# Optimization experiments

Hardware: AMD Instinct MI355X
Metric: run time of the kernel (lower is better)

The kernel has to match this reference:

```python
import jax, jax.numpy as jnp
import numpy as np

TEMP = 0.1
EPS = 1e-8  # torch cosine_similarity eps
B, P, N, D = 256, 32, 512, 256


def setup_inputs() -> dict:
    key = jax.random.key(0)
    k1, k2, k3 = jax.random.split(key, 3)
    return {
        "anchors": jax.random.normal(k1, (B, D), dtype=jnp.float32),
        "positives": jax.random.normal(k2, (B, P, D), dtype=jnp.float32),
        "negatives": jax.random.normal(k3, (B, N, D), dtype=jnp.float32),
    }


def reference(anchors, positives, negatives):
    # all_samples: (B, K, D) with K = P + N
    all_samples = jnp.concatenate([positives, negatives], axis=1)
    # Cosine similarity of anchor vs every sample (the original broadcasts the
    # anchor over P identical rows; we compute the (B, K) row once).
    dots = jnp.einsum("bd,bkd->bk", anchors, all_samples)          # (B, K)
    na = jnp.linalg.norm(anchors, axis=-1, keepdims=True)           # (B, 1)
    nk = jnp.linalg.norm(all_samples, axis=-1)                      # (B, K)
    sim = dots / jnp.maximum(na * nk, EPS) / TEMP                   # (B, K)
    logp = jax.nn.log_softmax(sim, axis=-1)                         # (B, K)
    p = positives.shape[1]
    # labels = arange(P): gather picks -log_softmax at column p for row p;
    # since all P rows equal, this is just the first P columns of logp.
    return -jnp.mean(logp[:, :p])
```

## Files before the change

### kernel.cpp

```cpp
#include <hip/hip_runtime.h>
#include <math.h>

#define TEMP_INV 10.0f
#define EPS 1e-8f
#define B_ 256
#define P_ 32
#define N_ 512
#define D_ 256
#define K_ (P_ + N_)

__device__ __forceinline__ float wave_reduce_sum(float v) {
    #pragma unroll
    for (int m = 32; m >= 1; m >>= 1) v += __shfl_xor(v, m, 64);
    return v;
}

__device__ __forceinline__ float wave_reduce_max(float v) {
    #pragma unroll
    for (int m = 32; m >= 1; m >>= 1) v = fmaxf(v, __shfl_xor(v, m, 64));
    return v;
}

__global__ __launch_bounds__(256) void sim_kernel(
    const float* __restrict__ anchors,
    const float* __restrict__ positives,
    const float* __restrict__ negatives,
    float* __restrict__ sim) {
    int gw   = blockIdx.x * 4 + (threadIdx.x >> 6);
    int lane = threadIdx.x & 63;
    if (gw >= B_ * K_) return;
    int b = gw / K_;
    int k = gw - b * K_;

    const float4* a4 = (const float4*)(anchors + (size_t)b * D_);
    const float4* s4 = (k < P_)
        ? (const float4*)(positives + ((size_t)b * P_ + k) * D_)
        : (const float4*)(negatives + ((size_t)b * N_ + (k - P_)) * D_);

    float4 a = a4[lane];
    float4 s = s4[lane];

    float dot = a.x * s.x + a.y * s.y + a.z * s.z + a.w * s.w;
    float ss  = s.x * s.x + s.y * s.y + s.z * s.z + s.w * s.w;
    float aa  = a.x * a.x + a.y * a.y + a.z * a.z + a.w * a.w;

    dot = wave_reduce_sum(dot);
    ss  = wave_reduce_sum(ss);
    aa  = wave_reduce_sum(aa);

    if (lane == 0) {
        float denom = fmaxf(sqrtf(aa) * sqrtf(ss), EPS);
        sim[gw] = dot / denom * TEMP_INV;
    }
}

__global__ __launch_bounds__(256) void softmax_kernel(
    const float* __restrict__ sim,
    float* __restrict__ partials) {
    int b    = blockIdx.x;
    int tid  = threadIdx.x;
    int wid  = tid >> 6;
    int lane = tid & 63;
    const float* row = sim + (size_t)b * K_;

    float vals[3];
    int cnt = 0;
    float lmax = -INFINITY;
    for (int k = tid; k < K_; k += 256) {
        float v = row[k];
        vals[cnt++] = v;
        lmax = fmaxf(lmax, v);
    }

    __shared__ float s_max[4];
    __shared__ float s_sum[4];
    __shared__ float s_pos[4];

    float wmax = wave_reduce_max(lmax);
    if (lane == 0) s_max[wid] = wmax;
    __syncthreads();
    float bmax = fmaxf(fmaxf(s_max[0], s_max[1]), fmaxf(s_max[2], s_max[3]));

    float lsum = 0.0f;
    for (int i = 0; i < cnt; i++) lsum += expf(vals[i] - bmax);
    float wsum = wave_reduce_sum(lsum);
    if (lane == 0) s_sum[wid] = wsum;

    float lp = (tid < P_) ? vals[0] : 0.0f;
    float wp = wave_reduce_sum(lp);
    if (lane == 0) s_pos[wid] = wp;
    __syncthreads();

    if (tid == 0) {
        float bsum = s_sum[0] + s_sum[1] + s_sum[2] + s_sum[3];
        float bpos = s_pos[0] + s_pos[1] + s_pos[2] + s_pos[3];
        float lse  = bmax + logf(bsum);
        partials[b] = (float)P_ * lse - bpos;
    }
}

__global__ __launch_bounds__(256) void finalize_kernel(
    const float* __restrict__ partials,
    float* __restrict__ out) {
    int tid  = threadIdx.x;
    int wid  = tid >> 6;
    int lane = tid & 63;
    float v  = partials[tid];
    float ws = wave_reduce_sum(v);
    __shared__ float s[4];
    if (lane == 0) s[wid] = ws;
    __syncthreads();
    if (tid == 0) {
        out[0] = (s[0] + s[1] + s[2] + s[3]) / (float)(B_ * P_);
    }
}

extern "C" void kernel_launch(void* const* d_in, const int* in_sizes, int n_in,
                              void* d_out, int out_size, void* d_ws, size_t ws_size,
                              hipStream_t stream) {
    const float* anchors   = (const float*)d_in[0];
    const float* positives = (const float*)d_in[1];
    const float* negatives = (const float*)d_in[2];
    float* out      = (float*)d_out;
    float* sim      = (float*)d_ws;
    float* partials = sim + (size_t)B_ * K_;

    int n_rows   = B_ * K_;
    int n_blocks = (n_rows + 3) / 4;
    sim_kernel<<<n_blocks, 256, 0, stream>>>(anchors, positives, negatives, sim);
    softmax_kernel<<<B_, 256, 0, stream>>>(sim, partials);
    finalize_kernel<<<1, 256, 0, stream>>>(partials, out);
}
```

Before: 202.1 us.

## Process four samples per wave and fold finalize into softmax via atomics

Each wave now computes cosine similarity for four consecutive samples, loading the anchor once and issuing four independent row loads. This cuts the block count fourfold, reuses the anchor and its norm, and gives more memory-level parallelism per wave. The finalize kernel is removed: the sim kernel zeroes the output and each softmax block atomically adds its scaled partial. The atomic accumulation makes the float summation order nondeterministic.

```diff
diff --git a/kernel.cpp b/kernel.cpp
--- a/kernel.cpp
+++ b/kernel.cpp
@@ -8,6 +8,7 @@
 #define N_ 512
 #define D_ 256
 #define K_ (P_ + N_)
+#define G_ (K_ / 4)
 
 __device__ __forceinline__ float wave_reduce_sum(float v) {
     #pragma unroll
@@ -21,42 +22,59 @@
     return v;
 }
 
+__device__ __forceinline__ float dot4(float4 a, float4 b) {
+    return a.x * b.x + a.y * b.y + a.z * b.z + a.w * b.w;
+}
+
 __global__ __launch_bounds__(256) void sim_kernel(
     const float* __restrict__ anchors,
     const float* __restrict__ positives,
     const float* __restrict__ negatives,
-    float* __restrict__ sim) {
+    float* __restrict__ sim,
+    float* __restrict__ out) {
     int gw   = blockIdx.x * 4 + (threadIdx.x >> 6);
     int lane = threadIdx.x & 63;
-    if (gw >= B_ * K_) return;
-    int b = gw / K_;
-    int k = gw - b * K_;
+    int b  = gw / G_;
+    int g  = gw - b * G_;
+    int k0 = g * 4;
 
     const float4* a4 = (const float4*)(anchors + (size_t)b * D_);
-    const float4* s4 = (k < P_)
-        ? (const float4*)(positives + ((size_t)b * P_ + k) * D_)
-        : (const float4*)(negatives + ((size_t)b * N_ + (k - P_)) * D_);
+    float4 a = a4[lane];
 
-    float4 a = a4[lane];
-    float4 s = s4[lane];
+    const float4* base = (k0 < P_)
+        ? (const float4*)(positives + ((size_t)b * P_ + k0) * D_)
+        : (const float4*)(negatives + ((size_t)b * N_ + (k0 - P_)) * D_);
 
-    float dot = a.x * s.x + a.y * s.y + a.z * s.z + a.w * s.w;
-    float ss  = s.x * s.x + s.y * s.y + s.z * s.z + s.w * s.w;
-    float aa  = a.x * a.x + a.y * a.y + a.z * a.z + a.w * a.w;
+    float4 s0 = base[lane];
+    float4 s1 = base[64 + lane];
+    float4 s2 = base[128 + lane];
+    float4 s3 = base[192 + lane];
 
-    dot = wave_reduce_sum(dot);
-    ss  = wave_reduce_sum(ss);
-    aa  = wave_reduce_sum(aa);
+    float na = sqrtf(wave_reduce_sum(dot4(a, a)));
+
+    float d0 = wave_reduce_sum(dot4(a, s0));
+    float q0 = wave_reduce_sum(dot4(s0, s0));
+    float d1 = wave_reduce_sum(dot4(a, s1));
+    float q1 = wave_reduce_sum(dot4(s1, s1));
+    float d2 = wave_reduce_sum(dot4(a, s2));
+    float q2 = wave_reduce_sum(dot4(s2, s2));
+    float d3 = wave_reduce_sum(dot4(a, s3));
+    float q3 = wave_reduce_sum(dot4(s3, s3));
 
     if (lane == 0) {
-        float denom = fmaxf(sqrtf(aa) * sqrtf(ss), EPS);
-        sim[gw] = dot / denom * TEMP_INV;
+        float* row = sim + (size_t)b * K_ + k0;
+        row[0] = d0 / fmaxf(na * sqrtf(q0), EPS) * TEMP_INV;
+        row[1] = d1 / fmaxf(na * sqrtf(q1), EPS) * TEMP_INV;
+        row[2] = d2 / fmaxf(na * sqrtf(q2), EPS) * TEMP_INV;
+        row[3] = d3 / fmaxf(na * sqrtf(q3), EPS) * TEMP_INV;
     }
+
+    if (blockIdx.x == 0 && threadIdx.x == 0) out[0] = 0.0f;
 }
 
 __global__ __launch_bounds__(256) void softmax_kernel(
     const float* __restrict__ sim,
-    float* __restrict__ partials) {
+    float* __restrict__ out) {
     int b    = blockIdx.x;
     int tid  = threadIdx.x;
     int wid  = tid >> 6;
@@ -95,23 +113,8 @@
         float bsum = s_sum[0] + s_sum[1] + s_sum[2] + s_sum[3];
         float bpos = s_pos[0] + s_pos[1] + s_pos[2] + s_pos[3];
         float lse  = bmax + logf(bsum);
-        partials[b] = (float)P_ * lse - bpos;
-    }
-}
-
-__global__ __launch_bounds__(256) void finalize_kernel(
-    const float* __restrict__ partials,
-    float* __restrict__ out) {
-    int tid  = threadIdx.x;
-    int wid  = tid >> 6;
-    int lane = tid & 63;
-    float v  = partials[tid];
-    float ws = wave_reduce_sum(v);
-    __shared__ float s[4];
-    if (lane == 0) s[wid] = ws;
-    __syncthreads();
-    if (tid == 0) {
-        out[0] = (s[0] + s[1] + s[2] + s[3]) / (float)(B_ * P_);
+        float partial = ((float)P_ * lse - bpos) * (1.0f / (float)(B_ * P_));
+        atomicAdd(out, partial);
     }
 }
 
@@ -121,13 +124,11 @@
     const float* anchors   = (const float*)d_in[0];
     const float* positives = (const float*)d_in[1];
     const float* negatives = (const float*)d_in[2];
-    float* out      = (float*)d_out;
-    float* sim      = (float*)d_ws;
-    float* partials = sim + (size_t)B_ * K_;
+    float* out = (float*)d_out;
+    float* sim = (float*)d_ws;
 
-    int n_rows   = B_ * K_;
-    int n_blocks = (n_rows + 3) / 4;
-    sim_kernel<<<n_blocks, 256, 0, stream>>>(anchors, positives, negatives, sim);
-    softmax_kernel<<<B_, 256, 0, stream>>>(sim, partials);
-    finalize_kernel<<<1, 256, 0, stream>>>(partials, out);
+    int n_waves  = B_ * G_;
+    int n_blocks = n_waves / 4;
+    sim_kernel<<<n_blocks, 256, 0, stream>>>(anchors, positives, negatives, sim, out);
+    softmax_kernel<<<B_, 256, 0, stream>>>(sim, out);
 }
```

Result: no change. 202.1 us, median of 2 (-0.0%).
